# Kernel tuning notes

Hardware: AMD Instinct MI355X
Metric: run time of the kernel (lower is better)

Reference implementation:

```python
import jax, jax.numpy as jnp
import numpy as np

# Dimensions inferred from the module (few-shot reweighted YOLOv2 region loss)
B, C, NA, NCPA = 64, 20, 5, 1          # batch, base classes, anchors, classes-per-anchor
H, W = 19, 19                           # feature map (608 input / stride 32)
T = 50                                  # cfg.max_boxes
THRESH = 0.6
COORD_SCALE = 1.0
CLASS_SCALE = 1.0
NB = B * C                              # per-class 'image' rows, as in the torch code
A4 = NA * H * W
EPS = 1e-12
BCE_EPS = 1e-7
ANCHORS = [[1.3221, 1.73145], [3.19275, 4.00944], [5.05587, 8.09892], [9.47112, 4.84053], [11.2364, 10.0071]]


def iou_xywh(x1, y1, w1, h1, x2, y2, w2, h2):
    # center-size IoU, matches darknet bbox_iou(x1y1x2y2=False)
    l = jnp.maximum(x1 - w1 * 0.5, x2 - w2 * 0.5)
    r = jnp.minimum(x1 + w1 * 0.5, x2 + w2 * 0.5)
    t = jnp.maximum(y1 - h1 * 0.5, y2 - h2 * 0.5)
    b = jnp.minimum(y1 + h1 * 0.5, y2 + h2 * 0.5)
    inter = jnp.clip(r - l, 0.0) * jnp.clip(b - t, 0.0)
    union = w1 * h1 + w2 * h2 - inter
    return inter / jnp.maximum(union, EPS)


def setup_inputs() -> dict:
    key = jax.random.key(0)
    k1, k2, k3, k4 = jax.random.split(key, 4)
    output = jax.random.normal(k1, (NB, NA * (5 + NCPA), H, W), jnp.float32) * 0.5
    # target rows: [cls, x, y, w, h] * T, coords in (0,1); x kept > 0 so all boxes are 'valid'
    cls_ids = jax.random.randint(k2, (B, C, T), 0, C).astype(jnp.float32)
    xy = jax.random.uniform(k3, (B, C, T, 2), minval=0.05, maxval=0.95)
    wh = jax.random.uniform(k4, (B, C, T, 2), minval=0.05, maxval=0.5)
    target = jnp.concatenate([cls_ids[..., None], xy, wh], axis=-1).reshape(B, C, T * 5)
    anchors = jnp.asarray(ANCHORS, jnp.float32)
    return {"output": output, "target": target, "anchors": anchors}


def _forward(output, target, anchors):
    target = jax.lax.stop_gradient(target)
    anchors = jax.lax.stop_gradient(anchors)
    out5 = output.reshape(NB, NA, 5 + NCPA, H, W)
    x = jax.nn.sigmoid(out5[:, :, 0])
    y = jax.nn.sigmoid(out5[:, :, 1])
    w = out5[:, :, 2]
    h = out5[:, :, 3]
    conf = jax.nn.sigmoid(out5[:, :, 4])
    # class logits regrouped to original batch: (B*NA*H*W, C)
    cls = out5[:, :, 5:5 + NCPA].reshape(NB, NA, H, W)
    cls_logits = cls.reshape(B, C, NA * H * W).transpose(0, 2, 1).reshape(-1, C)
    # decode pred boxes (detached, mirroring torch's use of .data)
    grid_x = jnp.arange(W, dtype=jnp.float32)[None, None, None, :]
    grid_y = jnp.arange(H, dtype=jnp.float32)[None, None, :, None]
    aw = anchors[:, 0][None, :, None, None]
    ah = anchors[:, 1][None, :, None, None]
    px = jax.lax.stop_gradient(x) + grid_x
    py = jax.lax.stop_gradient(y) + grid_y
    pw = jnp.exp(jax.lax.stop_gradient(w)) * aw
    ph = jnp.exp(jax.lax.stop_gradient(h)) * ah
    # ground-truth boxes per row
    tgt = target.reshape(NB, T, 5)
    cls_t = tgt[:, :, 0]
    gx = tgt[:, :, 1] * W
    gy = tgt[:, :, 2] * H
    gw = tgt[:, :, 3] * W
    gh = tgt[:, :, 4] * H
    # 'break on first zero x' semantics
    valid = jnp.cumprod((tgt[:, :, 1] != 0).astype(jnp.int32), axis=1) > 0
    # stage 1: zero conf_mask where any gt IoU > thresh (scan over T to avoid (NB,T,A4) blowup)
    pxf = px.reshape(NB, A4); pyf = py.reshape(NB, A4)
    pwf = pw.reshape(NB, A4); phf = ph.reshape(NB, A4)

    def iou_step(ci, xs):
        gxt, gyt, gwt, ght, vt = xs
        iou = iou_xywh(pxf, pyf, pwf, phf, gxt[:, None], gyt[:, None], gwt[:, None], ght[:, None])
        return jnp.maximum(ci, jnp.where(vt[:, None], iou, 0.0)), None

    cur_ious, _ = jax.lax.scan(iou_step, jnp.zeros((NB, A4), jnp.float32), (gx.T, gy.T, gw.T, gh.T, valid.T))
    conf_mask0 = jnp.where(cur_ious.reshape(NB, NA, H, W) > THRESH, 0.0, 1.0)
    # best anchor per gt by wh-only IoU
    inter = jnp.minimum(gw[..., None], anchors[:, 0]) * jnp.minimum(gh[..., None], anchors[:, 1])
    union = gw[..., None] * gh[..., None] + anchors[:, 0] * anchors[:, 1] - inter
    best_n = jnp.argmax(inter / jnp.maximum(union, EPS), axis=-1).astype(jnp.int32)  # (NB,T)
    gi = gx.astype(jnp.int32)
    gj = gy.astype(jnp.int32)
    # stage 2: ordered scatter of targets (later boxes overwrite earlier, as in the torch loops)
    binds = jnp.arange(NB)
    z = jnp.zeros((NB, NA, H, W), jnp.float32)
    # seen < 12800 branch: tx=ty=0.5, tw=th=0, coord_mask=1
    carry0 = (jnp.ones_like(z), z, conf_mask0, jnp.full_like(z, 0.5), jnp.full_like(z, 0.5), z, z, z, z)

    def tgt_step(carry, xs):
        cm, clm, cfm, tx, ty, tw, th, tconf, tcls = carry
        gxt, gyt, gwt, ght, bn, git, gjt, vt, ct = xs
        idx = (binds, bn, gjt, git)

        def upd(arr, val):
            return arr.at[idx].set(jnp.where(vt, val, arr[idx]))

        aw_b = anchors[bn, 0]
        ah_b = anchors[bn, 1]
        iou = iou_xywh(gxt, gyt, gwt, ght, px[idx], py[idx], pw[idx], ph[idx])
        cm = upd(cm, 1.0)
        clm = upd(clm, 1.0)
        cfm = upd(cfm, 1.0)
        tx = upd(tx, gxt - git.astype(jnp.float32))
        ty = upd(ty, gyt - gjt.astype(jnp.float32))
        tw = upd(tw, jnp.log(jnp.maximum(gwt, EPS) / aw_b))
        th = upd(th, jnp.log(jnp.maximum(ght, EPS) / ah_b))
        tconf = upd(tconf, iou)
        tcls = upd(tcls, ct)
        return (cm, clm, cfm, tx, ty, tw, th, tconf, tcls), None

    xs = (gx.T, gy.T, gw.T, gh.T, best_n.T, gi.T, gj.T, valid.T, cls_t.T)
    (coord_mask, cls_mask, conf_mask, tx, ty, tw, th, tconf, tcls), _ = jax.lax.scan(tgt_step, carry0, xs)
    # regroup per-class rows back to original batch (neg_ratio='full' -> counts[i] == C)
    cm_grp = cls_mask.reshape(B, C, NA, H, W).sum(axis=1)
    tcls_grp = tcls.reshape(B, C, NA, H, W).sum(axis=1)
    sel = (cm_grp == 1.0).reshape(-1)           # exclude colliding cells
    labels = tcls_grp.reshape(-1).astype(jnp.int32)

    def bce_mean(p, t):
        p = jnp.clip(p, BCE_EPS, 1.0 - BCE_EPS)
        return jnp.mean(-(t * jnp.log(p) + (1.0 - t) * jnp.log(1.0 - p)))

    loss_x = COORD_SCALE * bce_mean(x * coord_mask, tx * coord_mask)
    loss_y = COORD_SCALE * bce_mean(y * coord_mask, ty * coord_mask)
    loss_w = COORD_SCALE * 0.5 * jnp.mean((w * coord_mask - tw * coord_mask) ** 2)
    loss_h = COORD_SCALE * 0.5 * jnp.mean((h * coord_mask - th * coord_mask) ** 2)
    loss_conf = 0.5 * jnp.mean((conf * conf_mask - tconf * conf_mask) ** 2)
    logp = jax.nn.log_softmax(cls_logits, axis=-1)
    nll = -jnp.take_along_axis(logp, labels[:, None], axis=1)[:, 0]
    nsel = jnp.maximum(jnp.sum(sel.astype(jnp.float32)), 1.0)
    loss_cls = CLASS_SCALE * jnp.sum(jnp.where(sel, nll, 0.0)) / nsel
    return loss_x + loss_y + loss_w + loss_h + loss_conf + loss_cls


def reference(output, target, anchors):
    return _forward(output, target, anchors)
```

## Files before the change

kernel.cpp:

```cpp
#include <hip/hip_runtime.h>
#include <math.h>

constexpr int cB   = 64;
constexpr int cC   = 20;
constexpr int cNA  = 5;
constexpr int cH   = 19;
constexpr int cW   = 19;
constexpr int cT   = 50;
constexpr int cNB  = cB * cC;
constexpr int cHW  = cH * cW;
constexpr int cA4  = cNA * cHW;
constexpr int cCH  = cNA * 6;
constexpr long cNTOT = (long)cNB * cA4;
constexpr int cCLS_BLOCKS = cB * cNA;

__device__ __constant__ float cAW[cNA]   = {1.3221f, 3.19275f, 5.05587f, 9.47112f, 11.2364f};
__device__ __constant__ float cAH[cNA]   = {1.73145f, 4.00944f, 8.09892f, 4.84053f, 10.0071f};
__device__ __constant__ float cAREA[cNA] = {2.28930345f, 12.80114796f, 40.94706183f, 45.84455262f, 112.44377644f};
__device__ __constant__ float cLNAW[cNA] = {0.27920469f, 1.16088088f, 1.62060702f, 2.24822684f, 2.41915174f};
__device__ __constant__ float cLNAH[cNA] = {0.54896100f, 1.38865236f, 2.09173157f, 1.57701337f, 2.30329495f};

constexpr int ACC_BANKS = 64;
constexpr size_t OFF_CNT = 2560;
constexpr size_t OFF_ROW = 4096;
constexpr size_t ZERO_BYTES = OFF_ROW + (size_t)cB * cA4 * 4;
constexpr size_t OFF_GB4 = 466432;
constexpr size_t OFF_GB1 = OFF_GB4 + (size_t)cNB * cT * 16;
constexpr size_t WS_NEEDED = OFF_GB1 + (size_t)cNB * cT * 4;

__device__ __forceinline__ float fexp(float x) {
    return __builtin_amdgcn_exp2f(x * 1.4426950408889634f);
}
__device__ __forceinline__ float flog(float x) {
    return __builtin_amdgcn_logf(x) * 0.6931471805599453f;
}
__device__ __forceinline__ float frcp(float x) { return __builtin_amdgcn_rcpf(x); }
__device__ __forceinline__ float fsigmoid(float x) { return frcp(1.0f + fexp(-x)); }

typedef _Float16 h2 __attribute__((ext_vector_type(2)));
union HU { unsigned u; h2 h; };
__device__ __forceinline__ unsigned splat2(float v) {
    HU x; _Float16 f = (_Float16)v; x.h[0] = f; x.h[1] = f; return x.u;
}
constexpr float cS = 1.2649110640673518f;

__launch_bounds__(256)
__global__ void k_prep(const float* __restrict__ target, int* __restrict__ rowenc,
                       uint4* __restrict__ gb4, unsigned* __restrict__ gb1) {
    const int nb = blockIdx.x * 4 + (threadIdx.x >> 6);
    const int t  = threadIdx.x & 63;
    const int b_ = nb / cC;
    const int c_ = nb - b_ * cC;

    float xr = 1.f, yr = 0.f, wr = 0.f, hr = 0.f;
    const bool isT = (t < cT);
    if (isT) {
        const float* tg = target + (size_t)nb * (cT * 5) + t * 5;
        xr = tg[1]; yr = tg[2]; wr = tg[3]; hr = tg[4];
    }
    unsigned long long nz = __ballot(xr != 0.0f);
    bool valid = false;
    int cellv = -2 - t;
    if (isT) {
        unsigned long long below = (2ull << t) - 1ull;
        valid = ((~nz) & below) == 0ull;
        const int idx = nb * cT + t;
        float gx = xr * (float)cW, gy = yr * (float)cH;
        float gw = wr * (float)cW, gh = hr * (float)cH;
        uint4 bx;
        if (valid) {
            bx.x = splat2(cS * (gx - 0.5f * gw));
            bx.y = splat2(cS * (gx + 0.5f * gw));
            bx.z = splat2(cS * (gy - 0.5f * gh));
            bx.w = splat2(cS * (gy + 0.5f * gh));
            gb1[idx] = splat2(-0.6f * (gw * gh));
            float garea = gw * gh;
            float best = -1.0f; int bn = 0;
            for (int n = 0; n < cNA; ++n) {
                float inter = fminf(gw, cAW[n]) * fminf(gh, cAH[n]);
                float uni   = garea + cAREA[n] - inter;
                float r = inter / fmaxf(uni, 1e-12f);
                if (r > best) { best = r; bn = n; }
            }
            cellv = bn * cHW + (int)gy * cW + (int)gx;
        } else {
            bx.x = splat2(1e4f);  bx.y = splat2(-1e4f);
            bx.z = splat2(1e4f);  bx.w = splat2(-1e4f);
            gb1[idx] = splat2(0.0f);
        }
        gb4[idx] = bx;
    }
    bool loser = false;
    for (int i2 = 1; i2 < cT; ++i2) {
        int ci = __shfl(cellv, i2, 64);
        loser |= (i2 > t) && (ci == cellv);
    }
    if (valid && !loser)
        atomicAdd(&rowenc[b_ * cA4 + cellv], (1 << 10) | (c_ * cT + t));
}

template<bool GB>
__launch_bounds__(256)
__global__ void k_main(const float* __restrict__ outp, const float* __restrict__ target,
                       const uint4* __restrict__ gb4, const unsigned* __restrict__ gb1,
                       int* __restrict__ rowenc, double* __restrict__ acc) {
    __shared__ int s_win[1024];
    __shared__ float4 s_gt[cT];
    __shared__ int s_tc[cT];
    __shared__ __align__(16) unsigned s_box[cT][8];
    __shared__ double s_red[3][4];
    const int tid  = threadIdx.x;
    const int swz  = ((int)(blockIdx.x & 7)) * 320 + ((int)blockIdx.x >> 3);
    const int nb   = swz >> 1;
    const int half = swz & 1;
    const int winoff = half << 10;
    const int base = winoff + tid;
    const int b_   = nb / cC;
    const int c_   = nb - b_ * cC;
    const float* obase = outp + (size_t)nb * (cCH * cHW);
    const int nbT = nb * cT;

    s_win[tid] = -1; s_win[tid + 256] = -1;
    s_win[tid + 512] = -1; s_win[tid + 768] = -1;
    __syncthreads();

    if (tid < 64) {
        const int t = tid;
        float xr = 1.f, yr = 0.f, wr = 0.f, hr = 0.f;
        if (t < cT) {
            const float* tg = target + (size_t)nb * (cT * 5) + t * 5;
            xr = tg[1]; yr = tg[2]; wr = tg[3]; hr = tg[4];
        }
        unsigned long long nz = __ballot(xr != 0.0f);
        if (t < cT) {
            unsigned long long below = (2ull << t) - 1ull;
            bool valid = ((~nz) & below) == 0ull;
            float gx = xr * (float)cW, gy = yr * (float)cH;
            float gw = wr * (float)cW, gh = hr * (float)cH;
            s_gt[t] = make_float4(gx, gy, gw, gh);
            if (valid) {
                float garea = gw * gh;
                float best = -1.0f; int bn = 0;
                for (int n = 0; n < cNA; ++n) {
                    float inter = fminf(gw, cAW[n]) * fminf(gh, cAH[n]);
                    float uni   = garea + cAREA[n] - inter;
                    float r = inter / fmaxf(uni, 1e-12f);
                    if (r > best) { best = r; bn = n; }
                }
                int cell = bn * cHW + (int)gy * cW + (int)gx;
                if constexpr (!GB) {
                    s_tc[t] = cell;
                    s_box[t][0] = splat2(cS * (gx - 0.5f * gw));
                    s_box[t][1] = splat2(cS * (gx + 0.5f * gw));
                    s_box[t][2] = splat2(cS * (gy - 0.5f * gh));
                    s_box[t][3] = splat2(cS * (gy + 0.5f * gh));
                    s_box[t][4] = splat2(-0.6f * garea);
                }
                if (cell >= winoff && cell < winoff + 1024)
                    atomicMax(&s_win[cell - winoff], t);
            } else if constexpr (!GB) {
                s_tc[t] = -1;
                s_box[t][0] = splat2(1e4f);  s_box[t][1] = splat2(-1e4f);
                s_box[t][2] = splat2(1e4f);  s_box[t][3] = splat2(-1e4f);
                s_box[t][4] = splat2(0.0f);
            }
        }
    }
    __syncthreads();
    if constexpr (!GB) {
        if (tid < cT) {
            int cell = s_tc[tid];
            if (cell >= winoff && cell < winoff + 1024 && s_win[cell - winoff] == tid)
                atomicAdd(&rowenc[b_ * cA4 + cell], (1 << 10) | (c_ * cT + tid));
        }
    }

    h2 pl2[2], pr2[2], pt2[2], pb2[2], ov2[2], pa06h[2];
    float conf[4], tcf[4];
    unsigned wbits = 0;
    float bce = 0.0f, sq = 0.0f;
    const h2 z2 = { (_Float16)0.0f, (_Float16)0.0f };
    constexpr float cLN2 = 0.6931471805599453f;

    #pragma unroll
    for (int u = 0; u < 4; ++u) {
        int cell = base + (u << 8);
        bool a_  = cell < cA4;
        int cc   = a_ ? cell : (cA4 - 1);
        int na   = cc / cHW;
        int rem  = cc - na * cHW;
        int j    = rem / cW;
        int i    = rem - j * cW;
        const float* ob = obase + (size_t)(na * 6) * cHW + rem;
        float xl = ob[0], yl = ob[cHW], wl = ob[2*cHW], hl = ob[3*cHW], cl = ob[4*cHW];
        float Ex = __builtin_amdgcn_exp2f(-1.4426950408889634f * xl);
        float Sx = 1.0f + Ex;
        float x  = frcp(Sx);
        float Lx = __builtin_amdgcn_logf(Sx);
        float Ey = __builtin_amdgcn_exp2f(-1.4426950408889634f * yl);
        float Sy = 1.0f + Ey;
        float y  = frcp(Sy);
        float Ly = __builtin_amdgcn_logf(Sy);
        float cf = frcp(1.0f + fexp(-cl));
        float px = x + (float)i, py = y + (float)j;
        float pw = fexp(wl) * cAW[na], ph = fexp(hl) * cAH[na];
        float l0 = px - 0.5f*pw, r0 = px + 0.5f*pw;
        float t0 = py - 0.5f*ph, b0 = py + 0.5f*ph;
        float pa = pw * ph;
        int p = u >> 1, s = u & 1;
        pl2[p][s] = (_Float16)(cS * l0);  pr2[p][s] = (_Float16)(cS * r0);
        pt2[p][s] = (_Float16)(cS * t0);  pb2[p][s] = (_Float16)(cS * b0);
        pa06h[p][s] = (_Float16)(0.6f * pa);
        ov2[p][s] = (_Float16)0.0f;
        conf[u] = cf;

        float tx = 0.5f, ty = 0.5f, tw = 0.0f, th = 0.0f, tc = 0.0f;
        int wt = s_win[cc - winoff];
        bool wfl = (wt >= 0) && a_;
        if (wfl) {
            wbits |= (1u << u);
            float4 g = s_gt[wt];
            tx = g.x - (float)i;  ty = g.y - (float)j;
            tw = flog(fmaxf(g.z, 1e-12f)) - cLNAW[na];
            th = flog(fmaxf(g.w, 1e-12f)) - cLNAH[na];
            float iw = fminf(r0, g.x + 0.5f*g.z) - fmaxf(l0, g.x - 0.5f*g.z);
            float ih = fminf(b0, g.y + 0.5f*g.w) - fmaxf(t0, g.y - 0.5f*g.w);
            iw = fmaxf(iw, 0.0f); ih = fmaxf(ih, 0.0f);
            float inter = iw * ih;
            float uni   = g.z * g.w + pa - inter;
            tc = inter * frcp(fmaxf(uni, 1e-12f));
        }
        tcf[u] = tc;
        if (a_) {
            bce += (1.0f - tx) * xl + cLN2 * Lx;
            bce += (1.0f - ty) * yl + cLN2 * Ly;
            float dw = wl - tw, dh = hl - th;
            sq += dw*dw + dh*dh;
        }
    }

    #pragma unroll 10
    for (int t = 0; t < cT; ++t) {
        unsigned w0, w1, w2, w3, w4;
        if constexpr (GB) {
            uint4 bx = gb4[nbT + t];
            w0 = bx.x; w1 = bx.y; w2 = bx.z; w3 = bx.w;
            w4 = gb1[nbT + t];
        } else {
            uint4 bx = *(const uint4*)&s_box[t][0];
            w0 = bx.x; w1 = bx.y; w2 = bx.z; w3 = bx.w;
            w4 = s_box[t][4];
        }
        HU a, b, c, d, e;
        a.u = w0; b.u = w1; c.u = w2; d.u = w3; e.u = w4;
        #pragma unroll
        for (int p = 0; p < 2; ++p) {
            h2 iw = __builtin_elementwise_min(pr2[p], b.h) - __builtin_elementwise_max(pl2[p], a.h);
            h2 ih = __builtin_elementwise_min(pb2[p], d.h) - __builtin_elementwise_max(pt2[p], c.h);
            iw = __builtin_elementwise_max(iw, z2);
            ov2[p] = __builtin_elementwise_max(ov2[p], iw * ih + e.h);
        }
    }

    float sc = 0.0f;
    #pragma unroll
    for (int u = 0; u < 4; ++u) {
        int cell = base + (u << 8);
        if (cell >= cA4) continue;
        int p = u >> 1, s = u & 1;
        bool wfl  = (wbits >> u) & 1;
        bool over = ov2[p][s] > pa06h[p][s];
        float cm  = wfl ? 1.0f : (over ? 0.0f : 1.0f);
        float d   = (conf[u] - tcf[u]) * cm;
        sc += d * d;
    }

    double v0 = (double)bce, v1 = (double)sq, v2 = (double)sc;
    for (int off = 32; off > 0; off >>= 1) {
        v0 += __shfl_down(v0, off);
        v1 += __shfl_down(v1, off);
        v2 += __shfl_down(v2, off);
    }
    int lane = tid & 63, wid = tid >> 6;
    if (lane == 0) { s_red[0][wid] = v0; s_red[1][wid] = v1; s_red[2][wid] = v2; }
    __syncthreads();
    if (tid == 0) {
        double a0 = s_red[0][0] + s_red[0][1] + s_red[0][2] + s_red[0][3];
        double a1 = s_red[1][0] + s_red[1][1] + s_red[1][2] + s_red[1][3];
        double a2 = s_red[2][0] + s_red[2][1] + s_red[2][2] + s_red[2][3];
        int bank = blockIdx.x & (ACC_BANKS - 1);
        atomicAdd(&acc[0*ACC_BANKS + bank], a0);
        atomicAdd(&acc[1*ACC_BANKS + bank], a1);
        atomicAdd(&acc[2*ACC_BANKS + bank], a2);
    }
}

__launch_bounds__(384)
__global__ void k_cls(const float* __restrict__ outp, const float* __restrict__ target,
                      const int* __restrict__ rowenc, double* __restrict__ acc,
                      int* __restrict__ cnt, float* __restrict__ out) {
    __shared__ double s_red[2][6];
    __shared__ int s_last;
    const int tid = threadIdx.x;
    const int b   = blockIdx.x / cNA;
    const int na  = blockIdx.x - b * cNA;
    double nll = 0.0, ns = 0.0;
    if (tid < cHW) {
        const int rem = tid;
        const float* ob = outp + ((size_t)(b * cC) * cCH + na * 6 + 5) * cHW + rem;
        float l[cC]; float m = -1e30f;
        #pragma unroll
        for (int c = 0; c < cC; ++c) {
            l[c] = ob[(size_t)c * (cCH * cHW)];
            m = fmaxf(m, l[c]);
        }
        float s = 0.0f;
        #pragma unroll
        for (int c = 0; c < cC; ++c) s += fexp(l[c] - m);
        float lse = m + flog(s);
        int row = b * cA4 + na * cHW + rem;
        int v = rowenc[row];
        if ((v >> 10) == 1) {
            int payload = v & 1023;
            int selc = payload / cT;
            int selt = payload - selc * cT;
            int label = (int)target[((size_t)(b * cC + selc) * cT + selt) * 5];
            nll = (double)(lse - l[label]);
            ns  = 1.0;
        }
    }
    for (int off = 32; off > 0; off >>= 1) {
        nll += __shfl_down(nll, off);
        ns  += __shfl_down(ns, off);
    }
    int lane = tid & 63, wid = tid >> 6;
    if (lane == 0) { s_red[0][wid] = nll; s_red[1][wid] = ns; }
    __syncthreads();
    if (tid == 0) {
        double a0 = 0.0, a1 = 0.0;
        #pragma unroll
        for (int w = 0; w < 6; ++w) { a0 += s_red[0][w]; a1 += s_red[1][w]; }
        int bank = blockIdx.x & (ACC_BANKS - 1);
        atomicAdd(&acc[3*ACC_BANKS + bank], a0);
        atomicAdd(&acc[4*ACC_BANKS + bank], a1);
        __threadfence();
        s_last = (atomicAdd(cnt, 1) == cCLS_BLOCKS - 1);
    }
    __syncthreads();
    if (s_last && tid < 64) {
        __threadfence();
        double s[5];
        #pragma unroll
        for (int j = 0; j < 5; ++j) {
            double v = atomicAdd(&acc[j * ACC_BANKS + tid], 0.0);
            for (int off = 32; off > 0; off >>= 1) v += __shfl_down(v, off);
            s[j] = v;
        }
        if (tid == 0) {
            double Ninv = 1.0 / (double)cNTOT;
            double loss = s[0] * Ninv
                        + 0.5 * s[1] * Ninv
                        + 0.5 * s[2] * Ninv
                        + s[3] / fmax(s[4], 1.0);
            out[0] = (float)loss;
        }
    }
}

extern "C" void kernel_launch(void* const* d_in, const int* in_sizes, int n_in,
                              void* d_out, int out_size, void* d_ws, size_t ws_size,
                              hipStream_t stream) {
    const float* output = (const float*)d_in[0];
    const float* target = (const float*)d_in[1];
    char* ws = (char*)d_ws;
    double*   acc    = (double*)ws;
    int*      cnt    = (int*)(ws + OFF_CNT);
    int*      rowenc = (int*)(ws + OFF_ROW);
    uint4*    gb4    = (uint4*)(ws + OFF_GB4);
    unsigned* gb1    = (unsigned*)(ws + OFF_GB1);

    hipMemsetAsync(ws, 0, ZERO_BYTES, stream);

    if (ws_size >= WS_NEEDED) {
        k_prep<<<cNB / 4, 256, 0, stream>>>(target, rowenc, gb4, gb1);
        k_main<true><<<cNB * 2, 256, 0, stream>>>(output, target, gb4, gb1, rowenc, acc);
    } else {
        k_main<false><<<cNB * 2, 256, 0, stream>>>(output, target, gb4, gb1, rowenc, acc);
    }
    k_cls<<<cCLS_BLOCKS, 384, 0, stream>>>(output, target, rowenc, acc, cnt, (float*)d_out);
}
```

Before: 131.9 us.

## Process whole row per block in k_main and repartition k_cls into 256-thread chunks

k_main now uses one block per row covering all 1805 cells, 8 per thread, instead of two half-row blocks with 4 cells each. This drops the swizzled block mapping, so the per-row GT setup (target loads, anchor matching, the shared winner table) is done once per row instead of twice. k_cls is re-split into 8 chunks of 226 cells per batch with 256 threads instead of one 384-thread block per anchor. The trade-offs are more registers per thread in k_main, half as many blocks (less latency hiding), and a different grid shape for k_cls.

```diff
diff --git a/kernel.cpp b/kernel.cpp
--- a/kernel.cpp
+++ b/kernel.cpp
@@ -12,7 +12,8 @@
 constexpr int cA4  = cNA * cHW;
 constexpr int cCH  = cNA * 6;
 constexpr long cNTOT = (long)cNB * cA4;
-constexpr int cCLS_BLOCKS = cB * cNA;
+constexpr int cCLS_CHUNK  = 226;
+constexpr int cCLS_BLOCKS = cB * 8;
 
 __device__ __constant__ float cAW[cNA]   = {1.3221f, 3.19275f, 5.05587f, 9.47112f, 11.2364f};
 __device__ __constant__ float cAH[cNA]   = {1.73145f, 4.00944f, 8.09892f, 4.84053f, 10.0071f};
@@ -104,24 +105,19 @@
 __global__ void k_main(const float* __restrict__ outp, const float* __restrict__ target,
                        const uint4* __restrict__ gb4, const unsigned* __restrict__ gb1,
                        int* __restrict__ rowenc, double* __restrict__ acc) {
-    __shared__ int s_win[1024];
+    __shared__ int s_win[cA4];
     __shared__ float4 s_gt[cT];
     __shared__ int s_tc[cT];
-    __shared__ __align__(16) unsigned s_box[cT][8];
+    __shared__ __align__(16) unsigned s_box[GB ? 1 : cT][8];
     __shared__ double s_red[3][4];
-    const int tid  = threadIdx.x;
-    const int swz  = ((int)(blockIdx.x & 7)) * 320 + ((int)blockIdx.x >> 3);
-    const int nb   = swz >> 1;
-    const int half = swz & 1;
-    const int winoff = half << 10;
-    const int base = winoff + tid;
-    const int b_   = nb / cC;
-    const int c_   = nb - b_ * cC;
+    const int tid = threadIdx.x;
+    const int nb  = blockIdx.x;
+    const int b_  = nb / cC;
+    const int c_  = nb - b_ * cC;
     const float* obase = outp + (size_t)nb * (cCH * cHW);
     const int nbT = nb * cT;
 
-    s_win[tid] = -1; s_win[tid + 256] = -1;
-    s_win[tid + 512] = -1; s_win[tid + 768] = -1;
+    for (int k = tid; k < cA4; k += 256) s_win[k] = -1;
     __syncthreads();
 
     if (tid < 64) {
@@ -156,8 +152,7 @@
                     s_box[t][3] = splat2(cS * (gy + 0.5f * gh));
                     s_box[t][4] = splat2(-0.6f * garea);
                 }
-                if (cell >= winoff && cell < winoff + 1024)
-                    atomicMax(&s_win[cell - winoff], t);
+                atomicMax(&s_win[cell], t);
             } else if constexpr (!GB) {
                 s_tc[t] = -1;
                 s_box[t][0] = splat2(1e4f);  s_box[t][1] = splat2(-1e4f);
@@ -170,21 +165,21 @@
     if constexpr (!GB) {
         if (tid < cT) {
             int cell = s_tc[tid];
-            if (cell >= winoff && cell < winoff + 1024 && s_win[cell - winoff] == tid)
+            if (cell >= 0 && s_win[cell] == tid)
                 atomicAdd(&rowenc[b_ * cA4 + cell], (1 << 10) | (c_ * cT + tid));
         }
     }
 
-    h2 pl2[2], pr2[2], pt2[2], pb2[2], ov2[2], pa06h[2];
-    float conf[4], tcf[4];
+    h2 pl2[4], pr2[4], pt2[4], pb2[4], ov2[4], pa06h[4];
+    float conf[8], tcf[8];
     unsigned wbits = 0;
     float bce = 0.0f, sq = 0.0f;
     const h2 z2 = { (_Float16)0.0f, (_Float16)0.0f };
     constexpr float cLN2 = 0.6931471805599453f;
 
     #pragma unroll
-    for (int u = 0; u < 4; ++u) {
-        int cell = base + (u << 8);
+    for (int u = 0; u < 8; ++u) {
+        int cell = tid + (u << 8);
         bool a_  = cell < cA4;
         int cc   = a_ ? cell : (cA4 - 1);
         int na   = cc / cHW;
@@ -215,7 +210,7 @@
         conf[u] = cf;
 
         float tx = 0.5f, ty = 0.5f, tw = 0.0f, th = 0.0f, tc = 0.0f;
-        int wt = s_win[cc - winoff];
+        int wt = s_win[cc];
         bool wfl = (wt >= 0) && a_;
         if (wfl) {
             wbits |= (1u << u);
@@ -254,7 +249,7 @@
         HU a, b, c, d, e;
         a.u = w0; b.u = w1; c.u = w2; d.u = w3; e.u = w4;
         #pragma unroll
-        for (int p = 0; p < 2; ++p) {
+        for (int p = 0; p < 4; ++p) {
             h2 iw = __builtin_elementwise_min(pr2[p], b.h) - __builtin_elementwise_max(pl2[p], a.h);
             h2 ih = __builtin_elementwise_min(pb2[p], d.h) - __builtin_elementwise_max(pt2[p], c.h);
             iw = __builtin_elementwise_max(iw, z2);
@@ -264,8 +259,8 @@
 
     float sc = 0.0f;
     #pragma unroll
-    for (int u = 0; u < 4; ++u) {
-        int cell = base + (u << 8);
+    for (int u = 0; u < 8; ++u) {
+        int cell = tid + (u << 8);
         if (cell >= cA4) continue;
         int p = u >> 1, s = u & 1;
         bool wfl  = (wbits >> u) & 1;
@@ -295,18 +290,20 @@
     }
 }
 
-__launch_bounds__(384)
+__launch_bounds__(256)
 __global__ void k_cls(const float* __restrict__ outp, const float* __restrict__ target,
                       const int* __restrict__ rowenc, double* __restrict__ acc,
                       int* __restrict__ cnt, float* __restrict__ out) {
-    __shared__ double s_red[2][6];
+    __shared__ double s_red[2][4];
     __shared__ int s_last;
     const int tid = threadIdx.x;
-    const int b   = blockIdx.x / cNA;
-    const int na  = blockIdx.x - b * cNA;
+    const int b   = blockIdx.x >> 3;
+    const int q   = blockIdx.x & 7;
+    const int cell = q * cCLS_CHUNK + tid;
     double nll = 0.0, ns = 0.0;
-    if (tid < cHW) {
-        const int rem = tid;
+    if (tid < cCLS_CHUNK && cell < cA4) {
+        const int na  = cell / cHW;
+        const int rem = cell - na * cHW;
         const float* ob = outp + ((size_t)(b * cC) * cCH + na * 6 + 5) * cHW + rem;
         float l[cC]; float m = -1e30f;
         #pragma unroll
@@ -318,8 +315,7 @@
         #pragma unroll
         for (int c = 0; c < cC; ++c) s += fexp(l[c] - m);
         float lse = m + flog(s);
-        int row = b * cA4 + na * cHW + rem;
-        int v = rowenc[row];
+        int v = rowenc[b * cA4 + cell];
         if ((v >> 10) == 1) {
             int payload = v & 1023;
             int selc = payload / cT;
@@ -337,9 +333,8 @@
     if (lane == 0) { s_red[0][wid] = nll; s_red[1][wid] = ns; }
     __syncthreads();
     if (tid == 0) {
-        double a0 = 0.0, a1 = 0.0;
-        #pragma unroll
-        for (int w = 0; w < 6; ++w) { a0 += s_red[0][w]; a1 += s_red[1][w]; }
+        double a0 = s_red[0][0] + s_red[0][1] + s_red[0][2] + s_red[0][3];
+        double a1 = s_red[1][0] + s_red[1][1] + s_red[1][2] + s_red[1][3];
         int bank = blockIdx.x & (ACC_BANKS - 1);
         atomicAdd(&acc[3*ACC_BANKS + bank], a0);
         atomicAdd(&acc[4*ACC_BANKS + bank], a1);
@@ -383,9 +378,9 @@
 
     if (ws_size >= WS_NEEDED) {
         k_prep<<<cNB / 4, 256, 0, stream>>>(target, rowenc, gb4, gb1);
-        k_main<true><<<cNB * 2, 256, 0, stream>>>(output, target, gb4, gb1, rowenc, acc);
+        k_main<true><<<cNB, 256, 0, stream>>>(output, target, gb4, gb1, rowenc, acc);
     } else {
-        k_main<false><<<cNB * 2, 256, 0, stream>>>(output, target, gb4, gb1, rowenc, acc);
-    }
-    k_cls<<<cCLS_BLOCKS, 384, 0, stream>>>(output, target, rowenc, acc, cnt, (float*)d_out);
-}
+        k_main<false><<<cNB, 256, 0, stream>>>(output, target, gb4, gb1, rowenc, acc);
+    }
+    k_cls<<<cCLS_BLOCKS, 256, 0, stream>>>(output, target, rowenc, acc, cnt, (float*)d_out);
+}
```

Result: slower. 141.2 us (+7.0%).

## Fuse memset, prep, main and class kernels into one cooperative persistent kernel

Applied to the files above, without the earlier changes.

Replaces the memset plus three separate kernel launches with a single cooperative persistent kernel that uses grid-wide syncs between phases: zeroing and box precompute, then winner encoding and the main loss loop, then the class NLL, then the final reduction. The class phase becomes one wave per 64 rows instead of 384-thread blocks. This removes launch overhead and the memset, at the cost of grid-sync latency, an occupancy-limited grid that loops over tiles, and a fallback that silently returns when the workspace is too small.

```diff
diff --git a/kernel.cpp b/kernel.cpp
--- a/kernel.cpp
+++ b/kernel.cpp
@@ -1,5 +1,8 @@
 #include <hip/hip_runtime.h>
+#include <hip/hip_cooperative_groups.h>
 #include <math.h>
+
+namespace cg = cooperative_groups;
 
 constexpr int cB   = 64;
 constexpr int cC   = 20;
@@ -12,7 +15,8 @@
 constexpr int cA4  = cNA * cHW;
 constexpr int cCH  = cNA * 6;
 constexpr long cNTOT = (long)cNB * cA4;
-constexpr int cCLS_BLOCKS = cB * cNA;
+constexpr int cROW_INT4 = (cB * cA4) / 4;
+constexpr int cCLS_WAVES = (cB * cA4) / 64;
 
 __device__ __constant__ float cAW[cNA]   = {1.3221f, 3.19275f, 5.05587f, 9.47112f, 11.2364f};
 __device__ __constant__ float cAH[cNA]   = {1.73145f, 4.00944f, 8.09892f, 4.84053f, 10.0071f};
@@ -21,11 +25,10 @@
 __device__ __constant__ float cLNAH[cNA] = {0.54896100f, 1.38865236f, 2.09173157f, 1.57701337f, 2.30329495f};
 
 constexpr int ACC_BANKS = 64;
-constexpr size_t OFF_CNT = 2560;
 constexpr size_t OFF_ROW = 4096;
-constexpr size_t ZERO_BYTES = OFF_ROW + (size_t)cB * cA4 * 4;
-constexpr size_t OFF_GB4 = 466432;
-constexpr size_t OFF_GB1 = OFF_GB4 + (size_t)cNB * cT * 16;
+constexpr size_t OFF_GB4 = OFF_ROW + (size_t)cB * cA4 * 4;
+constexpr size_t OFF_GB4A = 466432;
+constexpr size_t OFF_GB1 = OFF_GB4A + (size_t)cNB * cT * 16;
 constexpr size_t WS_NEEDED = OFF_GB1 + (size_t)cNB * cT * 4;
 
 __device__ __forceinline__ float fexp(float x) {
@@ -35,7 +38,6 @@
     return __builtin_amdgcn_logf(x) * 0.6931471805599453f;
 }
 __device__ __forceinline__ float frcp(float x) { return __builtin_amdgcn_rcpf(x); }
-__device__ __forceinline__ float fsigmoid(float x) { return frcp(1.0f + fexp(-x)); }
 
 typedef _Float16 h2 __attribute__((ext_vector_type(2)));
 union HU { unsigned u; h2 h; };
@@ -44,101 +46,77 @@
 }
 constexpr float cS = 1.2649110640673518f;
 
-__launch_bounds__(256)
-__global__ void k_prep(const float* __restrict__ target, int* __restrict__ rowenc,
-                       uint4* __restrict__ gb4, unsigned* __restrict__ gb1) {
-    const int nb = blockIdx.x * 4 + (threadIdx.x >> 6);
-    const int t  = threadIdx.x & 63;
-    const int b_ = nb / cC;
-    const int c_ = nb - b_ * cC;
-
-    float xr = 1.f, yr = 0.f, wr = 0.f, hr = 0.f;
-    const bool isT = (t < cT);
-    if (isT) {
-        const float* tg = target + (size_t)nb * (cT * 5) + t * 5;
-        xr = tg[1]; yr = tg[2]; wr = tg[3]; hr = tg[4];
-    }
-    unsigned long long nz = __ballot(xr != 0.0f);
-    bool valid = false;
-    int cellv = -2 - t;
-    if (isT) {
-        unsigned long long below = (2ull << t) - 1ull;
-        valid = ((~nz) & below) == 0ull;
-        const int idx = nb * cT + t;
-        float gx = xr * (float)cW, gy = yr * (float)cH;
-        float gw = wr * (float)cW, gh = hr * (float)cH;
-        uint4 bx;
-        if (valid) {
-            bx.x = splat2(cS * (gx - 0.5f * gw));
-            bx.y = splat2(cS * (gx + 0.5f * gw));
-            bx.z = splat2(cS * (gy - 0.5f * gh));
-            bx.w = splat2(cS * (gy + 0.5f * gh));
-            gb1[idx] = splat2(-0.6f * (gw * gh));
-            float garea = gw * gh;
-            float best = -1.0f; int bn = 0;
-            for (int n = 0; n < cNA; ++n) {
-                float inter = fminf(gw, cAW[n]) * fminf(gh, cAH[n]);
-                float uni   = garea + cAREA[n] - inter;
-                float r = inter / fmaxf(uni, 1e-12f);
-                if (r > best) { best = r; bn = n; }
-            }
-            cellv = bn * cHW + (int)gy * cW + (int)gx;
-        } else {
-            bx.x = splat2(1e4f);  bx.y = splat2(-1e4f);
-            bx.z = splat2(1e4f);  bx.w = splat2(-1e4f);
-            gb1[idx] = splat2(0.0f);
-        }
-        gb4[idx] = bx;
-    }
-    bool loser = false;
-    for (int i2 = 1; i2 < cT; ++i2) {
-        int ci = __shfl(cellv, i2, 64);
-        loser |= (i2 > t) && (ci == cellv);
-    }
-    if (valid && !loser)
-        atomicAdd(&rowenc[b_ * cA4 + cellv], (1 << 10) | (c_ * cT + t));
-}
-
-template<bool GB>
-__launch_bounds__(256)
-__global__ void k_main(const float* __restrict__ outp, const float* __restrict__ target,
-                       const uint4* __restrict__ gb4, const unsigned* __restrict__ gb1,
-                       int* __restrict__ rowenc, double* __restrict__ acc) {
+__launch_bounds__(256, 8)
+__global__ void k_fused(const float* __restrict__ outp, const float* __restrict__ target,
+                        int* rowenc, uint4* gb4, unsigned* gb1,
+                        double* acc, float* out) {
     __shared__ int s_win[1024];
     __shared__ float4 s_gt[cT];
-    __shared__ int s_tc[cT];
-    __shared__ __align__(16) unsigned s_box[cT][8];
     __shared__ double s_red[3][4];
     const int tid  = threadIdx.x;
-    const int swz  = ((int)(blockIdx.x & 7)) * 320 + ((int)blockIdx.x >> 3);
-    const int nb   = swz >> 1;
-    const int half = swz & 1;
-    const int winoff = half << 10;
-    const int base = winoff + tid;
-    const int b_   = nb / cC;
-    const int c_   = nb - b_ * cC;
-    const float* obase = outp + (size_t)nb * (cCH * cHW);
-    const int nbT = nb * cT;
-
-    s_win[tid] = -1; s_win[tid + 256] = -1;
-    s_win[tid + 512] = -1; s_win[tid + 768] = -1;
-    __syncthreads();
-
-    if (tid < 64) {
-        const int t = tid;
+    const int bid  = blockIdx.x;
+    const int G    = gridDim.x;
+    const int wid  = tid >> 6;
+    const int lane = tid & 63;
+    const int wslot = bid * 4 + wid;
+    const int WTOT  = G * 4;
+
+    {
+        const int gtid = bid * 256 + tid;
+        const int NTH  = G * 256;
+        int4 z4; z4.x = z4.y = z4.z = z4.w = 0;
+        int4* r4 = (int4*)rowenc;
+        for (int k = gtid; k < cROW_INT4; k += NTH) r4[k] = z4;
+        for (int k = gtid; k < 5 * ACC_BANKS; k += NTH) acc[k] = 0.0;
+
+        for (int nb = wslot; nb < cNB; nb += WTOT) {
+            float xr = 1.f, yr = 0.f, wr = 0.f, hr = 0.f;
+            const bool isT = lane < cT;
+            if (isT) {
+                const float* tg = target + (size_t)nb * (cT * 5) + lane * 5;
+                xr = tg[1]; yr = tg[2]; wr = tg[3]; hr = tg[4];
+            }
+            unsigned long long nz = __ballot(xr != 0.0f);
+            if (isT) {
+                unsigned long long below = (2ull << lane) - 1ull;
+                bool valid = ((~nz) & below) == 0ull;
+                const int idx = nb * cT + lane;
+                float gx = xr * (float)cW, gy = yr * (float)cH;
+                float gw = wr * (float)cW, gh = hr * (float)cH;
+                uint4 bx;
+                if (valid) {
+                    bx.x = splat2(cS * (gx - 0.5f * gw));
+                    bx.y = splat2(cS * (gx + 0.5f * gw));
+                    bx.z = splat2(cS * (gy - 0.5f * gh));
+                    bx.w = splat2(cS * (gy + 0.5f * gh));
+                    gb1[idx] = splat2(-0.6f * (gw * gh));
+                } else {
+                    bx.x = splat2(1e4f);  bx.y = splat2(-1e4f);
+                    bx.z = splat2(1e4f);  bx.w = splat2(-1e4f);
+                    gb1[idx] = splat2(0.0f);
+                }
+                gb4[idx] = bx;
+            }
+        }
+    }
+    cg::this_grid().sync();
+
+    for (int nb = wslot; nb < cNB; nb += WTOT) {
+        const int b_ = nb / cC, c_ = nb - b_ * cC;
         float xr = 1.f, yr = 0.f, wr = 0.f, hr = 0.f;
-        if (t < cT) {
-            const float* tg = target + (size_t)nb * (cT * 5) + t * 5;
+        const bool isT = lane < cT;
+        if (isT) {
+            const float* tg = target + (size_t)nb * (cT * 5) + lane * 5;
             xr = tg[1]; yr = tg[2]; wr = tg[3]; hr = tg[4];
         }
         unsigned long long nz = __ballot(xr != 0.0f);
-        if (t < cT) {
-            unsigned long long below = (2ull << t) - 1ull;
-            bool valid = ((~nz) & below) == 0ull;
-            float gx = xr * (float)cW, gy = yr * (float)cH;
-            float gw = wr * (float)cW, gh = hr * (float)cH;
-            s_gt[t] = make_float4(gx, gy, gw, gh);
+        bool valid = false; int cellv = -2 - lane;
+        if (isT) {
+            unsigned long long below = (2ull << lane) - 1ull;
+            valid = ((~nz) & below) == 0ull;
             if (valid) {
+                float gx = xr * (float)cW, gy = yr * (float)cH;
+                float gw = wr * (float)cW, gh = hr * (float)cH;
                 float garea = gw * gh;
                 float best = -1.0f; int bn = 0;
                 for (int n = 0; n < cNA; ++n) {
@@ -147,214 +125,223 @@
                     float r = inter / fmaxf(uni, 1e-12f);
                     if (r > best) { best = r; bn = n; }
                 }
-                int cell = bn * cHW + (int)gy * cW + (int)gx;
-                if constexpr (!GB) {
-                    s_tc[t] = cell;
-                    s_box[t][0] = splat2(cS * (gx - 0.5f * gw));
-                    s_box[t][1] = splat2(cS * (gx + 0.5f * gw));
-                    s_box[t][2] = splat2(cS * (gy - 0.5f * gh));
-                    s_box[t][3] = splat2(cS * (gy + 0.5f * gh));
-                    s_box[t][4] = splat2(-0.6f * garea);
+                cellv = bn * cHW + (int)gy * cW + (int)gx;
+            }
+        }
+        bool loser = false;
+        for (int i2 = 1; i2 < cT; ++i2) {
+            int ci = __shfl(cellv, i2, 64);
+            loser |= (i2 > lane) && (ci == cellv);
+        }
+        if (valid && !loser)
+            atomicAdd(&rowenc[b_ * cA4 + cellv], (1 << 10) | (c_ * cT + lane));
+    }
+
+    for (int j = bid; j < cNB * 2; j += G) {
+        const int it   = (j & 7) * 320 + (j >> 3);
+        const int nb   = it >> 1;
+        const int half = it & 1;
+        const int winoff = half << 10;
+        const int base = winoff + tid;
+        const float* obase = outp + (size_t)nb * (cCH * cHW);
+        const int nbT = nb * cT;
+
+        s_win[tid] = -1; s_win[tid + 256] = -1;
+        s_win[tid + 512] = -1; s_win[tid + 768] = -1;
+        __syncthreads();
+
+        if (tid < 64) {
+            const int t = tid;
+            float xr = 1.f, yr = 0.f, wr = 0.f, hr = 0.f;
+            if (t < cT) {
+                const float* tg = target + (size_t)nb * (cT * 5) + t * 5;
+                xr = tg[1]; yr = tg[2]; wr = tg[3]; hr = tg[4];
+            }
+            unsigned long long nz = __ballot(xr != 0.0f);
+            if (t < cT) {
+                unsigned long long below = (2ull << t) - 1ull;
+                bool valid = ((~nz) & below) == 0ull;
+                float gx = xr * (float)cW, gy = yr * (float)cH;
+                float gw = wr * (float)cW, gh = hr * (float)cH;
+                s_gt[t] = make_float4(gx, gy, gw, gh);
+                if (valid) {
+                    float garea = gw * gh;
+                    float best = -1.0f; int bn = 0;
+                    for (int n = 0; n < cNA; ++n) {
+                        float inter = fminf(gw, cAW[n]) * fminf(gh, cAH[n]);
+                        float uni   = garea + cAREA[n] - inter;
+                        float r = inter / fmaxf(uni, 1e-12f);
+                        if (r > best) { best = r; bn = n; }
+                    }
+                    int cell = bn * cHW + (int)gy * cW + (int)gx;
+                    if (cell >= winoff && cell < winoff + 1024)
+                        atomicMax(&s_win[cell - winoff], t);
                 }
-                if (cell >= winoff && cell < winoff + 1024)
-                    atomicMax(&s_win[cell - winoff], t);
-            } else if constexpr (!GB) {
-                s_tc[t] = -1;
-                s_box[t][0] = splat2(1e4f);  s_box[t][1] = splat2(-1e4f);
-                s_box[t][2] = splat2(1e4f);  s_box[t][3] = splat2(-1e4f);
-                s_box[t][4] = splat2(0.0f);
-            }
-        }
-    }
-    __syncthreads();
-    if constexpr (!GB) {
-        if (tid < cT) {
-            int cell = s_tc[tid];
-            if (cell >= winoff && cell < winoff + 1024 && s_win[cell - winoff] == tid)
-                atomicAdd(&rowenc[b_ * cA4 + cell], (1 << 10) | (c_ * cT + tid));
-        }
-    }
-
-    h2 pl2[2], pr2[2], pt2[2], pb2[2], ov2[2], pa06h[2];
-    float conf[4], tcf[4];
-    unsigned wbits = 0;
-    float bce = 0.0f, sq = 0.0f;
-    const h2 z2 = { (_Float16)0.0f, (_Float16)0.0f };
-    constexpr float cLN2 = 0.6931471805599453f;
-
-    #pragma unroll
-    for (int u = 0; u < 4; ++u) {
-        int cell = base + (u << 8);
-        bool a_  = cell < cA4;
-        int cc   = a_ ? cell : (cA4 - 1);
-        int na   = cc / cHW;
-        int rem  = cc - na * cHW;
-        int j    = rem / cW;
-        int i    = rem - j * cW;
-        const float* ob = obase + (size_t)(na * 6) * cHW + rem;
-        float xl = ob[0], yl = ob[cHW], wl = ob[2*cHW], hl = ob[3*cHW], cl = ob[4*cHW];
-        float Ex = __builtin_amdgcn_exp2f(-1.4426950408889634f * xl);
-        float Sx = 1.0f + Ex;
-        float x  = frcp(Sx);
-        float Lx = __builtin_amdgcn_logf(Sx);
-        float Ey = __builtin_amdgcn_exp2f(-1.4426950408889634f * yl);
-        float Sy = 1.0f + Ey;
-        float y  = frcp(Sy);
-        float Ly = __builtin_amdgcn_logf(Sy);
-        float cf = frcp(1.0f + fexp(-cl));
-        float px = x + (float)i, py = y + (float)j;
-        float pw = fexp(wl) * cAW[na], ph = fexp(hl) * cAH[na];
-        float l0 = px - 0.5f*pw, r0 = px + 0.5f*pw;
-        float t0 = py - 0.5f*ph, b0 = py + 0.5f*ph;
-        float pa = pw * ph;
-        int p = u >> 1, s = u & 1;
-        pl2[p][s] = (_Float16)(cS * l0);  pr2[p][s] = (_Float16)(cS * r0);
-        pt2[p][s] = (_Float16)(cS * t0);  pb2[p][s] = (_Float16)(cS * b0);
-        pa06h[p][s] = (_Float16)(0.6f * pa);
-        ov2[p][s] = (_Float16)0.0f;
-        conf[u] = cf;
-
-        float tx = 0.5f, ty = 0.5f, tw = 0.0f, th = 0.0f, tc = 0.0f;
-        int wt = s_win[cc - winoff];
-        bool wfl = (wt >= 0) && a_;
-        if (wfl) {
-            wbits |= (1u << u);
-            float4 g = s_gt[wt];
-            tx = g.x - (float)i;  ty = g.y - (float)j;
-            tw = flog(fmaxf(g.z, 1e-12f)) - cLNAW[na];
-            th = flog(fmaxf(g.w, 1e-12f)) - cLNAH[na];
-            float iw = fminf(r0, g.x + 0.5f*g.z) - fmaxf(l0, g.x - 0.5f*g.z);
-            float ih = fminf(b0, g.y + 0.5f*g.w) - fmaxf(t0, g.y - 0.5f*g.w);
-            iw = fmaxf(iw, 0.0f); ih = fmaxf(ih, 0.0f);
-            float inter = iw * ih;
-            float uni   = g.z * g.w + pa - inter;
-            tc = inter * frcp(fmaxf(uni, 1e-12f));
-        }
-        tcf[u] = tc;
-        if (a_) {
-            bce += (1.0f - tx) * xl + cLN2 * Lx;
-            bce += (1.0f - ty) * yl + cLN2 * Ly;
-            float dw = wl - tw, dh = hl - th;
-            sq += dw*dw + dh*dh;
-        }
-    }
-
-    #pragma unroll 10
-    for (int t = 0; t < cT; ++t) {
-        unsigned w0, w1, w2, w3, w4;
-        if constexpr (GB) {
-            uint4 bx = gb4[nbT + t];
-            w0 = bx.x; w1 = bx.y; w2 = bx.z; w3 = bx.w;
-            w4 = gb1[nbT + t];
-        } else {
-            uint4 bx = *(const uint4*)&s_box[t][0];
-            w0 = bx.x; w1 = bx.y; w2 = bx.z; w3 = bx.w;
-            w4 = s_box[t][4];
-        }
-        HU a, b, c, d, e;
-        a.u = w0; b.u = w1; c.u = w2; d.u = w3; e.u = w4;
+            }
+        }
+        __syncthreads();
+
+        h2 pl2[2], pr2[2], pt2[2], pb2[2], ov2[2], pa06h[2];
+        float conf[4], tcf[4];
+        unsigned wbits = 0;
+        float bce = 0.0f, sq = 0.0f;
+        const h2 z2 = { (_Float16)0.0f, (_Float16)0.0f };
+        constexpr float cLN2 = 0.6931471805599453f;
+
         #pragma unroll
-        for (int p = 0; p < 2; ++p) {
-            h2 iw = __builtin_elementwise_min(pr2[p], b.h) - __builtin_elementwise_max(pl2[p], a.h);
-            h2 ih = __builtin_elementwise_min(pb2[p], d.h) - __builtin_elementwise_max(pt2[p], c.h);
-            iw = __builtin_elementwise_max(iw, z2);
-            ov2[p] = __builtin_elementwise_max(ov2[p], iw * ih + e.h);
-        }
-    }
-
-    float sc = 0.0f;
-    #pragma unroll
-    for (int u = 0; u < 4; ++u) {
-        int cell = base + (u << 8);
-        if (cell >= cA4) continue;
-        int p = u >> 1, s = u & 1;
-        bool wfl  = (wbits >> u) & 1;
-        bool over = ov2[p][s] > pa06h[p][s];
-        float cm  = wfl ? 1.0f : (over ? 0.0f : 1.0f);
-        float d   = (conf[u] - tcf[u]) * cm;
-        sc += d * d;
-    }
-
-    double v0 = (double)bce, v1 = (double)sq, v2 = (double)sc;
-    for (int off = 32; off > 0; off >>= 1) {
-        v0 += __shfl_down(v0, off);
-        v1 += __shfl_down(v1, off);
-        v2 += __shfl_down(v2, off);
-    }
-    int lane = tid & 63, wid = tid >> 6;
-    if (lane == 0) { s_red[0][wid] = v0; s_red[1][wid] = v1; s_red[2][wid] = v2; }
-    __syncthreads();
-    if (tid == 0) {
-        double a0 = s_red[0][0] + s_red[0][1] + s_red[0][2] + s_red[0][3];
-        double a1 = s_red[1][0] + s_red[1][1] + s_red[1][2] + s_red[1][3];
-        double a2 = s_red[2][0] + s_red[2][1] + s_red[2][2] + s_red[2][3];
-        int bank = blockIdx.x & (ACC_BANKS - 1);
-        atomicAdd(&acc[0*ACC_BANKS + bank], a0);
-        atomicAdd(&acc[1*ACC_BANKS + bank], a1);
-        atomicAdd(&acc[2*ACC_BANKS + bank], a2);
-    }
-}
-
-__launch_bounds__(384)
-__global__ void k_cls(const float* __restrict__ outp, const float* __restrict__ target,
-                      const int* __restrict__ rowenc, double* __restrict__ acc,
-                      int* __restrict__ cnt, float* __restrict__ out) {
-    __shared__ double s_red[2][6];
-    __shared__ int s_last;
-    const int tid = threadIdx.x;
-    const int b   = blockIdx.x / cNA;
-    const int na  = blockIdx.x - b * cNA;
-    double nll = 0.0, ns = 0.0;
-    if (tid < cHW) {
-        const int rem = tid;
-        const float* ob = outp + ((size_t)(b * cC) * cCH + na * 6 + 5) * cHW + rem;
-        float l[cC]; float m = -1e30f;
+        for (int u = 0; u < 4; ++u) {
+            int cell = base + (u << 8);
+            bool a_  = cell < cA4;
+            int cc   = a_ ? cell : (cA4 - 1);
+            int na   = cc / cHW;
+            int rem  = cc - na * cHW;
+            int jj   = rem / cW;
+            int ii   = rem - jj * cW;
+            const float* ob = obase + (size_t)(na * 6) * cHW + rem;
+            float xl = ob[0], yl = ob[cHW], wl = ob[2*cHW], hl = ob[3*cHW], cl = ob[4*cHW];
+            float Ex = __builtin_amdgcn_exp2f(-1.4426950408889634f * xl);
+            float Sx = 1.0f + Ex;
+            float x  = frcp(Sx);
+            float Lx = __builtin_amdgcn_logf(Sx);
+            float Ey = __builtin_amdgcn_exp2f(-1.4426950408889634f * yl);
+            float Sy = 1.0f + Ey;
+            float y  = frcp(Sy);
+            float Ly = __builtin_amdgcn_logf(Sy);
+            float cf = frcp(1.0f + fexp(-cl));
+            float px = x + (float)ii, py = y + (float)jj;
+            float pw = fexp(wl) * cAW[na], ph = fexp(hl) * cAH[na];
+            float l0 = px - 0.5f*pw, r0 = px + 0.5f*pw;
+            float t0 = py - 0.5f*ph, b0 = py + 0.5f*ph;
+            float pa = pw * ph;
+            int p = u >> 1, s = u & 1;
+            pl2[p][s] = (_Float16)(cS * l0);  pr2[p][s] = (_Float16)(cS * r0);
+            pt2[p][s] = (_Float16)(cS * t0);  pb2[p][s] = (_Float16)(cS * b0);
+            pa06h[p][s] = (_Float16)(0.6f * pa);
+            ov2[p][s] = (_Float16)0.0f;
+            conf[u] = cf;
+
+            float tx = 0.5f, ty = 0.5f, tw = 0.0f, th = 0.0f, tc = 0.0f;
+            int wt = s_win[cc - winoff];
+            bool wfl = (wt >= 0) && a_;
+            if (wfl) {
+                wbits |= (1u << u);
+                float4 g = s_gt[wt];
+                tx = g.x - (float)ii;  ty = g.y - (float)jj;
+                tw = flog(fmaxf(g.z, 1e-12f)) - cLNAW[na];
+                th = flog(fmaxf(g.w, 1e-12f)) - cLNAH[na];
+                float iw = fminf(r0, g.x + 0.5f*g.z) - fmaxf(l0, g.x - 0.5f*g.z);
+                float ih = fminf(b0, g.y + 0.5f*g.w) - fmaxf(t0, g.y - 0.5f*g.w);
+                iw = fmaxf(iw, 0.0f); ih = fmaxf(ih, 0.0f);
+                float inter = iw * ih;
+                float uni   = g.z * g.w + pa - inter;
+                tc = inter * frcp(fmaxf(uni, 1e-12f));
+            }
+            tcf[u] = tc;
+            if (a_) {
+                bce += (1.0f - tx) * xl + cLN2 * Lx;
+                bce += (1.0f - ty) * yl + cLN2 * Ly;
+                float dw = wl - tw, dh = hl - th;
+                sq += dw*dw + dh*dh;
+            }
+        }
+
+        #pragma unroll 10
+        for (int t = 0; t < cT; ++t) {
+            uint4 bx    = gb4[nbT + t];
+            unsigned gv = gb1[nbT + t];
+            HU a, b, c, d, e;
+            a.u = bx.x; b.u = bx.y; c.u = bx.z; d.u = bx.w; e.u = gv;
+            #pragma unroll
+            for (int p = 0; p < 2; ++p) {
+                h2 iw = __builtin_elementwise_min(pr2[p], b.h) - __builtin_elementwise_max(pl2[p], a.h);
+                h2 ih = __builtin_elementwise_min(pb2[p], d.h) - __builtin_elementwise_max(pt2[p], c.h);
+                iw = __builtin_elementwise_max(iw, z2);
+                ov2[p] = __builtin_elementwise_max(ov2[p], iw * ih + e.h);
+            }
+        }
+
+        float sc = 0.0f;
         #pragma unroll
-        for (int c = 0; c < cC; ++c) {
-            l[c] = ob[(size_t)c * (cCH * cHW)];
-            m = fmaxf(m, l[c]);
-        }
-        float s = 0.0f;
-        #pragma unroll
-        for (int c = 0; c < cC; ++c) s += fexp(l[c] - m);
-        float lse = m + flog(s);
-        int row = b * cA4 + na * cHW + rem;
-        int v = rowenc[row];
-        if ((v >> 10) == 1) {
-            int payload = v & 1023;
-            int selc = payload / cT;
-            int selt = payload - selc * cT;
-            int label = (int)target[((size_t)(b * cC + selc) * cT + selt) * 5];
-            nll = (double)(lse - l[label]);
-            ns  = 1.0;
-        }
-    }
-    for (int off = 32; off > 0; off >>= 1) {
-        nll += __shfl_down(nll, off);
-        ns  += __shfl_down(ns, off);
-    }
-    int lane = tid & 63, wid = tid >> 6;
-    if (lane == 0) { s_red[0][wid] = nll; s_red[1][wid] = ns; }
-    __syncthreads();
-    if (tid == 0) {
-        double a0 = 0.0, a1 = 0.0;
-        #pragma unroll
-        for (int w = 0; w < 6; ++w) { a0 += s_red[0][w]; a1 += s_red[1][w]; }
-        int bank = blockIdx.x & (ACC_BANKS - 1);
-        atomicAdd(&acc[3*ACC_BANKS + bank], a0);
-        atomicAdd(&acc[4*ACC_BANKS + bank], a1);
-        __threadfence();
-        s_last = (atomicAdd(cnt, 1) == cCLS_BLOCKS - 1);
-    }
-    __syncthreads();
-    if (s_last && tid < 64) {
-        __threadfence();
+        for (int u = 0; u < 4; ++u) {
+            int cell = base + (u << 8);
+            if (cell >= cA4) continue;
+            int p = u >> 1, s = u & 1;
+            bool wfl  = (wbits >> u) & 1;
+            bool over = ov2[p][s] > pa06h[p][s];
+            float cm  = wfl ? 1.0f : (over ? 0.0f : 1.0f);
+            float d   = (conf[u] - tcf[u]) * cm;
+            sc += d * d;
+        }
+
+        double v0 = (double)bce, v1 = (double)sq, v2 = (double)sc;
+        for (int off = 32; off > 0; off >>= 1) {
+            v0 += __shfl_down(v0, off);
+            v1 += __shfl_down(v1, off);
+            v2 += __shfl_down(v2, off);
+        }
+        if (lane == 0) { s_red[0][wid] = v0; s_red[1][wid] = v1; s_red[2][wid] = v2; }
+        __syncthreads();
+        if (tid == 0) {
+            double a0 = s_red[0][0] + s_red[0][1] + s_red[0][2] + s_red[0][3];
+            double a1 = s_red[1][0] + s_red[1][1] + s_red[1][2] + s_red[1][3];
+            double a2 = s_red[2][0] + s_red[2][1] + s_red[2][2] + s_red[2][3];
+            int bank = it & (ACC_BANKS - 1);
+            atomicAdd(&acc[0*ACC_BANKS + bank], a0);
+            atomicAdd(&acc[1*ACC_BANKS + bank], a1);
+            atomicAdd(&acc[2*ACC_BANKS + bank], a2);
+        }
+    }
+    cg::this_grid().sync();
+
+    {
+        const int w2 = wid * G + bid;
+        if (w2 < cCLS_WAVES) {
+            const int g    = w2 * 64 + lane;
+            const int b    = g / cA4;
+            const int cell = g - b * cA4;
+            const int na   = cell / cHW;
+            const int rem  = cell - na * cHW;
+            const float* ob = outp + ((size_t)(b * cC) * cCH + na * 6 + 5) * cHW + rem;
+            float l[cC]; float m = -1e30f;
+            #pragma unroll
+            for (int c = 0; c < cC; ++c) {
+                l[c] = ob[(size_t)c * (cCH * cHW)];
+                m = fmaxf(m, l[c]);
+            }
+            float s = 0.0f;
+            #pragma unroll
+            for (int c = 0; c < cC; ++c) s += fexp(l[c] - m);
+            float lse = m + flog(s);
+            double nll = 0.0, ns = 0.0;
+            int v = rowenc[g];
+            if ((v >> 10) == 1) {
+                int payload = v & 1023;
+                int selc = payload / cT;
+                int selt = payload - selc * cT;
+                int label = (int)target[((size_t)(b * cC + selc) * cT + selt) * 5];
+                nll = (double)(lse - l[label]);
+                ns  = 1.0;
+            }
+            for (int off = 32; off > 0; off >>= 1) {
+                nll += __shfl_down(nll, off);
+                ns  += __shfl_down(ns, off);
+            }
+            if (lane == 0) {
+                int bank = w2 & (ACC_BANKS - 1);
+                atomicAdd(&acc[3*ACC_BANKS + bank], nll);
+                atomicAdd(&acc[4*ACC_BANKS + bank], ns);
+            }
+        }
+    }
+    cg::this_grid().sync();
+
+    if (bid == 0 && tid < 64) {
         double s[5];
         #pragma unroll
-        for (int j = 0; j < 5; ++j) {
-            double v = atomicAdd(&acc[j * ACC_BANKS + tid], 0.0);
+        for (int j2 = 0; j2 < 5; ++j2) {
+            double v = atomicAdd(&acc[j2 * ACC_BANKS + tid], 0.0);
             for (int off = 32; off > 0; off >>= 1) v += __shfl_down(v, off);
-            s[j] = v;
+            s[j2] = v;
         }
         if (tid == 0) {
             double Ninv = 1.0 / (double)cNTOT;
@@ -374,18 +361,26 @@
     const float* target = (const float*)d_in[1];
     char* ws = (char*)d_ws;
     double*   acc    = (double*)ws;
-    int*      cnt    = (int*)(ws + OFF_CNT);
     int*      rowenc = (int*)(ws + OFF_ROW);
-    uint4*    gb4    = (uint4*)(ws + OFF_GB4);
+    uint4*    gb4    = (uint4*)(ws + OFF_GB4A);
     unsigned* gb1    = (unsigned*)(ws + OFF_GB1);
-
-    hipMemsetAsync(ws, 0, ZERO_BYTES, stream);
-
-    if (ws_size >= WS_NEEDED) {
-        k_prep<<<cNB / 4, 256, 0, stream>>>(target, rowenc, gb4, gb1);
-        k_main<true><<<cNB * 2, 256, 0, stream>>>(output, target, gb4, gb1, rowenc, acc);
-    } else {
-        k_main<false><<<cNB * 2, 256, 0, stream>>>(output, target, gb4, gb1, rowenc, acc);
-    }
-    k_cls<<<cCLS_BLOCKS, 384, 0, stream>>>(output, target, rowenc, acc, cnt, (float*)d_out);
-}
+    float*    outp   = (float*)d_out;
+
+    if (ws_size < WS_NEEDED) return;
+
+    static int s_grid = 0;
+    if (s_grid == 0) {
+        int per = 0;
+        if (hipOccupancyMaxActiveBlocksPerMultiprocessor(
+                &per, (const void*)k_fused, 256, 0) != hipSuccess || per <= 0)
+            per = 4;
+        long g = (long)per * 256;
+        if (g > cNB * 2) g = cNB * 2;
+        s_grid = (int)g;
+    }
+
+    void* args[] = { (void*)&output, (void*)&target, (void*)&rowenc,
+                     (void*)&gb4, (void*)&gb1, (void*)&acc, (void*)&outp };
+    hipLaunchCooperativeKernel((const void*)k_fused, dim3(s_grid), dim3(256),
+                               args, 0, stream);
+}
```

Measured after the change: 494.2 us. 3.75x slower.
